# Kernel optimization log

Hardware: AMD Instinct MI355X
Metric: run time of the kernel (lower is better)

## Reference

```python
import jax, jax.numpy as jnp
import numpy as np

B, S, D_IN, D_OUT, R = 8, 2048, 4096, 4096, 16

def setup_inputs() -> dict:
    key = jax.random.key(0)
    k = jax.random.split(key, 7)
    return {
        "x": jax.random.normal(k[0], (B, S, D_IN), dtype=jnp.float32),
        "osora_U": jax.random.normal(k[1], (D_OUT, R), dtype=jnp.float32) * 0.02,
        "osora_V": jax.random.normal(k[2], (R, D_IN), dtype=jnp.float32) * 0.02,
        "osora_S": jax.random.normal(k[3], (R,), dtype=jnp.float32),
        "osora_O": jax.random.normal(k[4], (D_OUT,), dtype=jnp.float32),
        "magnitude": jax.random.uniform(k[5], (D_OUT,), dtype=jnp.float32) + 0.5,
        "base_weight": jax.random.normal(k[6], (D_OUT, D_IN), dtype=jnp.float32) * 0.02,
    }

def reference(x, osora_U, osora_V, osora_S, osora_O, magnitude, base_weight):
    # osora_weight = diag(O) @ U @ diag(S) @ V  -> [out, in]
    osora_weight = (osora_O[:, None] * (osora_U * osora_S[None, :])) @ osora_V
    # low-rank path applied to activations: x @ osora_weight.T  -> [B, S, out]
    osora_result = jnp.einsum('bsr,or->bso', jnp.einsum('bsi,ri->bsr', x, osora_V) * osora_S, osora_U) * osora_O
    # weight norm of (base + adapter) per output row; detached in the original
    weight_norm = jax.lax.stop_gradient(
        jnp.linalg.norm(base_weight + osora_weight, axis=1).astype(base_weight.dtype))
    mag_norm_scale = (magnitude / weight_norm)[None, None, :]  # broadcast over B, S
    base_out = jnp.einsum('bsi,oi->bso', x, base_weight)
    return (mag_norm_scale - 1.0) * base_out + mag_norm_scale * osora_result
```

## Files before the change

kernel.cpp:

```cpp
#include <hip/hip_runtime.h>


#define M_TOT 16384
#define N_TOT 4096
#define K_TOT 4096

typedef __attribute__((ext_vector_type(8))) short bf16x8;
typedef __attribute__((ext_vector_type(4))) float f32x4;

__device__ __forceinline__ unsigned short f2bf(float f){
  union { float f; unsigned int u; } v; v.f = f;
  unsigned int u = v.u;
  u += 0x7FFFu + ((u >> 16) & 1u);
  return (unsigned short)(u >> 16);
}

__device__ __forceinline__ void async_lds16(const void* g, void* l){
  __builtin_amdgcn_global_load_lds(
      (const __attribute__((address_space(1))) unsigned int*)g,
      (__attribute__((address_space(3))) unsigned int*)l, 16, 0, 0);
}

__global__ __launch_bounds__(256) void cast_f32_to_bf16_x4(
    const float* __restrict__ src, unsigned short* __restrict__ dst, int n4){
  int i = blockIdx.x * 256 + threadIdx.x;
  if (i >= n4) return;
  float4 v = ((const float4*)src)[i];
  ushort4 o;
  o.x = f2bf(v.x); o.y = f2bf(v.y); o.z = f2bf(v.z); o.w = f2bf(v.w);
  ((ushort4*)dst)[i] = o;
}

__global__ __launch_bounds__(256) void tgemm_kernel(
    const unsigned short* __restrict__ xb, const unsigned short* __restrict__ vb,
    unsigned short* __restrict__ tb){
  int lane = threadIdx.x & 63;
  int wave = threadIdx.x >> 6;
  int quad = lane >> 4;
  int r16  = lane & 15;
  int m0 = (blockIdx.x * 4 + wave) * 16;
  const unsigned short* xptr = xb + (m0 + r16) * K_TOT + quad * 8;
  const unsigned short* vptr = vb + r16 * K_TOT + quad * 8;
  f32x4 acc = {0.f, 0.f, 0.f, 0.f};
  for (int k = 0; k < K_TOT; k += 32){
    bf16x8 a = *(const bf16x8*)(xptr + k);
    bf16x8 b = *(const bf16x8*)(vptr + k);
    acc = __builtin_amdgcn_mfma_f32_16x16x32_bf16(a, b, acc, 0, 0, 0);
  }
  for (int reg = 0; reg < 4; reg++){
    int m = m0 + quad * 4 + reg;
    tb[m * 16 + r16] = f2bf(acc[reg]);
  }
}

__global__ __launch_bounds__(256) void norm_kernel(
    const float* __restrict__ bw, const float* __restrict__ U,
    const float* __restrict__ S, const float* __restrict__ O,
    const float* __restrict__ mag, const float* __restrict__ V,
    float* __restrict__ s_out, float* __restrict__ sm1_out,
    unsigned short* __restrict__ w2b){
  __shared__ float Vl[16 * 1024];
  __shared__ float C8[8 * 16];
  __shared__ float red[8 * 4];
  int t = threadIdx.x;
  int lane = t & 63, wave = t >> 6;
  int n0 = blockIdx.x * 8;
  if (t < 128){
    int row = t >> 4, r = t & 15;
    int n = n0 + row;
    float c = O[n] * S[r] * U[n * 16 + r];
    C8[t] = c;
    w2b[n * 16 + r] = f2bf(c);
  }
  float nsq[8];
  for (int i = 0; i < 8; i++) nsq[i] = 0.f;
  for (int ch = 0; ch < 4; ch++){
    __syncthreads();
    for (int j = 0; j < 16; j++){
      int idx4 = j * 256 + t;
      int r = idx4 >> 8, c4 = idx4 & 255;
      *(float4*)(Vl + r * 1024 + c4 * 4) =
          *(const float4*)(V + r * 4096 + ch * 1024 + c4 * 4);
    }
    __syncthreads();
    for (int row = 0; row < 8; row++){
      float4 b = *(const float4*)(bw + (n0 + row) * 4096 + ch * 1024 + t * 4);
      float a0 = 0.f, a1 = 0.f, a2 = 0.f, a3 = 0.f;
      for (int r = 0; r < 16; r++){
        float cr = C8[row * 16 + r];
        const float* vp = Vl + r * 1024 + t * 4;
        a0 += cr * vp[0]; a1 += cr * vp[1]; a2 += cr * vp[2]; a3 += cr * vp[3];
      }
      float d0 = b.x + a0, d1 = b.y + a1, d2 = b.z + a2, d3 = b.w + a3;
      nsq[row] += d0*d0 + d1*d1 + d2*d2 + d3*d3;
    }
  }
  for (int row = 0; row < 8; row++){
    float v = nsq[row];
    for (int off = 32; off > 0; off >>= 1) v += __shfl_down(v, off);
    if (lane == 0) red[row * 4 + wave] = v;
  }
  __syncthreads();
  if (t < 8){
    int n = n0 + t;
    float tot = red[t*4] + red[t*4+1] + red[t*4+2] + red[t*4+3];
    float s = mag[n] / sqrtf(tot);
    s_out[n] = s;
    sm1_out[n] = s - 1.0f;
  }
}

__global__ __launch_bounds__(256) void gemm_kernel(
    const unsigned short* __restrict__ A,
    const unsigned short* __restrict__ B,
    const unsigned short* __restrict__ Tb,
    const unsigned short* __restrict__ W2b,
    const float* __restrict__ s_arr, const float* __restrict__ sm1_arr,
    float* __restrict__ Cout){
  __shared__ unsigned short Al[128 * 64];
  __shared__ unsigned short Bl[128 * 64];
  int tid  = threadIdx.x;
  int lane = tid & 63;
  int wave = tid >> 6;
  int quad = lane >> 4;
  int r16  = lane & 15;
  int xm   = lane & 7;

  const int GM = 16, NBN = 32;
  int bidx  = blockIdx.x;
  int super = bidx / (GM * NBN);
  int rem   = bidx % (GM * NBN);
  int bm = super * GM + (rem & (GM - 1));
  int bn = rem / GM;
  int m0 = bm * 128;
  int n0 = bn * 128;

  int wm = (wave >> 1) * 64;
  int wn = (wave & 1) * 64;

  int a_goff[4], b_goff[4], l_off[4];
  for (int j = 0; j < 4; j++){
    int u = j * 256 + tid;
    int mrow = u >> 3;
    int ko = (u & 7) ^ (mrow & 7);
    a_goff[j] = (m0 + mrow) * K_TOT + ko * 8;
    b_goff[j] = (n0 + mrow) * K_TOT + ko * 8;
    l_off[j]  = u * 8;
  }
  int koff0 = (quad ^ xm) * 16;
  int koff1 = ((4 + quad) ^ xm) * 16;

  f32x4 zf = {0.f, 0.f, 0.f, 0.f};
  f32x4 acc[4][4];
  for (int i = 0; i < 4; i++)
    for (int j = 0; j < 4; j++) acc[i][j] = zf;

  for (int kk = 0; kk < K_TOT; kk += 64){
    __syncthreads();
    for (int j = 0; j < 4; j++){
      async_lds16(A + a_goff[j] + kk, Al + l_off[j]);
      async_lds16(B + b_goff[j] + kk, Bl + l_off[j]);
    }
    __syncthreads();
    for (int ks = 0; ks < 2; ks++){
      int ko = ks ? koff1 : koff0;
      bf16x8 af[4], bfr[4];
      for (int tm = 0; tm < 4; tm++)
        af[tm] = *(const bf16x8*)((const char*)Al + (wm + tm*16 + r16) * 128 + ko);
      for (int tn = 0; tn < 4; tn++)
        bfr[tn] = *(const bf16x8*)((const char*)Bl + (wn + tn*16 + r16) * 128 + ko);
      for (int tm = 0; tm < 4; tm++)
        for (int tn = 0; tn < 4; tn++)
          acc[tm][tn] = __builtin_amdgcn_mfma_f32_16x16x32_bf16(
              af[tm], bfr[tn], acc[tm][tn], 0, 0, 0);
    }
  }

  __syncthreads();
  {
    int row = tid >> 1, half = tid & 1;
    uint4 z = {0u, 0u, 0u, 0u};
    *(uint4*)(Al + row * 40 + half * 8)      = *(const uint4*)(Tb  + (m0 + row) * 16 + half * 8);
    *(uint4*)(Al + row * 40 + 16 + half * 8) = z;
    *(uint4*)(Bl + row * 40 + half * 8)      = *(const uint4*)(W2b + (n0 + row) * 16 + half * 8);
    *(uint4*)(Bl + row * 40 + 16 + half * 8) = z;
  }
  __syncthreads();
  for (int tn = 0; tn < 4; tn++){
    int nn = n0 + wn + tn * 16 + r16;
    float s   = s_arr[nn];
    float sm1 = sm1_arr[nn];
    bf16x8 b2 = *(const bf16x8*)(Bl + (wn + tn*16 + r16) * 40 + quad * 8);
    for (int tm = 0; tm < 4; tm++){
      bf16x8 a2 = *(const bf16x8*)(Al + (wm + tm*16 + r16) * 40 + quad * 8);
      f32x4 o2 = __builtin_amdgcn_mfma_f32_16x16x32_bf16(a2, b2, zf, 0, 0, 0);
      int mbase = m0 + wm + tm * 16 + quad * 4;
      float* cp = Cout + (long)mbase * N_TOT + nn;
      cp[0]         = sm1 * acc[tm][tn][0] + s * o2[0];
      cp[N_TOT]     = sm1 * acc[tm][tn][1] + s * o2[1];
      cp[2 * N_TOT] = sm1 * acc[tm][tn][2] + s * o2[2];
      cp[3 * N_TOT] = sm1 * acc[tm][tn][3] + s * o2[3];
    }
  }
}

extern "C" void kernel_launch(void* const* d_in, const int* in_sizes, int n_in,
                              void* d_out, int out_size, void* d_ws, size_t ws_size,
                              hipStream_t stream){
  const float* x   = (const float*)d_in[0];
  const float* U   = (const float*)d_in[1];
  const float* V   = (const float*)d_in[2];
  const float* S   = (const float*)d_in[3];
  const float* O   = (const float*)d_in[4];
  const float* mag = (const float*)d_in[5];
  const float* bw  = (const float*)d_in[6];
  float* out = (float*)d_out;

  char* ws = (char*)d_ws;
  unsigned short* xb  = (unsigned short*)(ws);
  unsigned short* wb  = (unsigned short*)(ws + 134217728);
  unsigned short* vb  = (unsigned short*)(ws + 167772160);
  unsigned short* tb  = (unsigned short*)(ws + 167903232);
  unsigned short* w2b = (unsigned short*)(ws + 168427520);
  float* s_arr   = (float*)(ws + 168558592);
  float* sm1_arr = (float*)(ws + 168574976);
  (void)in_sizes; (void)n_in; (void)out_size; (void)ws_size;

  cast_f32_to_bf16_x4<<<16384, 256, 0, stream>>>(bw, wb, 4194304);
  cast_f32_to_bf16_x4<<<64,    256, 0, stream>>>(V,  vb, 16384);
  cast_f32_to_bf16_x4<<<65536, 256, 0, stream>>>(x,  xb, 16777216);
  tgemm_kernel<<<256, 256, 0, stream>>>(xb, vb, tb);
  norm_kernel<<<512, 256, 0, stream>>>(bw, U, S, O, mag, V, s_arr, sm1_arr, w2b);
  gemm_kernel<<<4096, 256, 0, stream>>>(xb, wb, tb, w2b, s_arr, sm1_arr, out);
}
```

Before: 1.271 ms.

## Rewrite main GEMM as 256x256 tile with double-buffered ping-pong LDS pipeline

The fused GEMM moves from 128x128 tiles with 4 waves to 256x256 tiles with 8 waves. LDS is double-buffered, and async global-to-LDS loads for the next K-step are issued between MFMA clusters. Explicit vmcnt/lgkmcnt waits, barriers and s_setprio interleave memory traffic with MFMA work, and the block order is remapped for L2 reuse. The aim is to hide global-load latency and raise arithmetic intensity. The cost is 128KB of LDS per block, many barriers, and high register pressure from the 8x4 accumulator array.

After: 1.081 ms. 15.0% less time.

```diff
diff --git a/kernel.cpp b/kernel.cpp
--- a/kernel.cpp
+++ b/kernel.cpp
@@ -110,98 +110,169 @@
   }
 }
 
-__global__ __launch_bounds__(256) void gemm_kernel(
+__global__ __launch_bounds__(512, 2) void gemm_kernel(
     const unsigned short* __restrict__ A,
     const unsigned short* __restrict__ B,
     const unsigned short* __restrict__ Tb,
     const unsigned short* __restrict__ W2b,
     const float* __restrict__ s_arr, const float* __restrict__ sm1_arr,
     float* __restrict__ Cout){
-  __shared__ unsigned short Al[128 * 64];
-  __shared__ unsigned short Bl[128 * 64];
+  __shared__ unsigned short AL[2][16384];
+  __shared__ unsigned short BL[2][16384];
   int tid  = threadIdx.x;
   int lane = tid & 63;
   int wave = tid >> 6;
+  int wm   = wave >> 2;
+  int wn   = wave & 3;
   int quad = lane >> 4;
   int r16  = lane & 15;
-  int xm   = lane & 7;
-
-  const int GM = 16, NBN = 32;
-  int bidx  = blockIdx.x;
-  int super = bidx / (GM * NBN);
-  int rem   = bidx % (GM * NBN);
-  int bm = super * GM + (rem & (GM - 1));
-  int bn = rem / GM;
-  int m0 = bm * 128;
-  int n0 = bn * 128;
-
-  int wm = (wave >> 1) * 64;
-  int wn = (wave & 1) * 64;
-
-  int a_goff[4], b_goff[4], l_off[4];
-  for (int j = 0; j < 4; j++){
-    int u = j * 256 + tid;
-    int mrow = u >> 3;
-    int ko = (u & 7) ^ (mrow & 7);
-    a_goff[j] = (m0 + mrow) * K_TOT + ko * 8;
-    b_goff[j] = (n0 + mrow) * K_TOT + ko * 8;
-    l_off[j]  = u * 8;
-  }
-  int koff0 = (quad ^ xm) * 16;
-  int koff1 = ((4 + quad) ^ xm) * 16;
+  int xm   = r16 & 7;
+
+  int bid = blockIdx.x;
+  int id  = (bid & 7) * 128 + (bid >> 3);
+  int bm = id >> 4, bn = id & 15;
+  int m0 = bm * 256, n0 = bn * 256;
+
+  int urow0 = tid >> 3,         uslot0 = tid & 7;
+  int urow1 = (512+tid) >> 3,   uslot1 = (512+tid) & 7;
+  int ko0 = uslot0 ^ (urow0 & 7);
+  int ko1 = uslot1 ^ (urow1 & 7);
+  int a_src0 = (m0 + urow0) * K_TOT + ko0 * 8;
+  int a_src1 = (m0 + urow1) * K_TOT + ko1 * 8;
+  int b_src0 = (n0 + urow0) * K_TOT + ko0 * 8;
+  int b_src1 = (n0 + urow1) * K_TOT + ko1 * 8;
+  int l_u0 = tid * 8;
+  int l_u1 = (512 + tid) * 8;
+  const int HSTEP = 128 * K_TOT;
+
+#define STG_A(bf_, h_, kt_) do{ \
+    async_lds16(A + a_src0 + (h_)*HSTEP + (kt_)*64, &AL[bf_][(h_)*8192 + l_u0]); \
+    async_lds16(A + a_src1 + (h_)*HSTEP + (kt_)*64, &AL[bf_][(h_)*8192 + l_u1]); }while(0)
+#define STG_B(bf_, h_, kt_) do{ \
+    async_lds16(B + b_src0 + (h_)*HSTEP + (kt_)*64, &BL[bf_][(h_)*8192 + l_u0]); \
+    async_lds16(B + b_src1 + (h_)*HSTEP + (kt_)*64, &BL[bf_][(h_)*8192 + l_u1]); }while(0)
+
+#define BAR()   __builtin_amdgcn_s_barrier()
+#define LGKM0() asm volatile("s_waitcnt lgkmcnt(0)" ::: "memory")
+#define VMW(n_) asm volatile("s_waitcnt vmcnt(" #n_ ")" ::: "memory")
+
+  int a_row = (wm * 128 + r16) * 64;
+  int b_row = (wn * 64  + r16) * 64;
+  int koA[2] = { (quad ^ xm) * 8, ((4 + quad) ^ xm) * 8 };
 
   f32x4 zf = {0.f, 0.f, 0.f, 0.f};
-  f32x4 acc[4][4];
-  for (int i = 0; i < 4; i++)
+  f32x4 acc[8][4];
+#pragma unroll
+  for (int i = 0; i < 8; i++)
+#pragma unroll
     for (int j = 0; j < 4; j++) acc[i][j] = zf;
-
-  for (int kk = 0; kk < K_TOT; kk += 64){
-    __syncthreads();
-    for (int j = 0; j < 4; j++){
-      async_lds16(A + a_goff[j] + kk, Al + l_off[j]);
-      async_lds16(B + b_goff[j] + kk, Bl + l_off[j]);
-    }
-    __syncthreads();
-    for (int ks = 0; ks < 2; ks++){
-      int ko = ks ? koff1 : koff0;
-      bf16x8 af[4], bfr[4];
-      for (int tm = 0; tm < 4; tm++)
-        af[tm] = *(const bf16x8*)((const char*)Al + (wm + tm*16 + r16) * 128 + ko);
-      for (int tn = 0; tn < 4; tn++)
-        bfr[tn] = *(const bf16x8*)((const char*)Bl + (wn + tn*16 + r16) * 128 + ko);
-      for (int tm = 0; tm < 4; tm++)
-        for (int tn = 0; tn < 4; tn++)
-          acc[tm][tn] = __builtin_amdgcn_mfma_f32_16x16x32_bf16(
-              af[tm], bfr[tn], acc[tm][tn], 0, 0, 0);
-    }
-  }
-
+  bf16x8 af[4][2], bA[2][2], bB[2][2];
+
+#define RD_A(bf_, mb_) do{ _Pragma("unroll") \
+    for (int mf = 0; mf < 4; ++mf){ _Pragma("unroll") \
+      for (int ks = 0; ks < 2; ++ks) \
+        af[mf][ks] = *(const bf16x8*)(&AL[bf_][a_row + ((mb_)+mf)*1024 + koA[ks]]); } }while(0)
+#define RD_B(bf_, dst_, nb_) do{ _Pragma("unroll") \
+    for (int nf = 0; nf < 2; ++nf){ _Pragma("unroll") \
+      for (int ks = 0; ks < 2; ++ks) \
+        dst_[nf][ks] = *(const bf16x8*)(&BL[bf_][b_row + ((nb_)+nf)*1024 + koA[ks]]); } }while(0)
+#define MMQ(mb_, bset_, nb_) do{ _Pragma("unroll") \
+    for (int ks = 0; ks < 2; ++ks){ _Pragma("unroll") \
+      for (int mf = 0; mf < 4; ++mf){ _Pragma("unroll") \
+        for (int nf = 0; nf < 2; ++nf) \
+          acc[(mb_)+mf][(nb_)+nf] = __builtin_amdgcn_mfma_f32_16x16x32_bf16( \
+              af[mf][ks], bset_[nf][ks], acc[(mb_)+mf][(nb_)+nf], 0, 0, 0); } } }while(0)
+
+  STG_A(0, 0, 0); STG_A(0, 1, 0); STG_B(0, 0, 0); STG_B(0, 1, 0);
+  STG_B(1, 0, 1); STG_B(1, 1, 1); STG_A(1, 0, 1);
+  VMW(6);
+  BAR();
+
+#pragma unroll 1
+  for (int i = 0; i < 32; ++i){
+    int kt = 2 * i;
+    int pf = (i < 31);
+
+    RD_A(0, 0); RD_B(0, bA, 0);
+    STG_A(1, 1, kt + 1);
+    BAR(); LGKM0();
+    __builtin_amdgcn_s_setprio(1); MMQ(0, bA, 0); __builtin_amdgcn_s_setprio(0);
+    BAR();
+    RD_B(0, bB, 2);
+    BAR(); LGKM0();
+    __builtin_amdgcn_s_setprio(1); MMQ(0, bB, 2); __builtin_amdgcn_s_setprio(0);
+    BAR();
+    RD_A(0, 4);
+    if (pf) STG_B(0, 0, kt + 2);
+    BAR(); LGKM0();
+    __builtin_amdgcn_s_setprio(1); MMQ(4, bA, 0); __builtin_amdgcn_s_setprio(0);
+    BAR();
+    if (pf) STG_B(0, 1, kt + 2);
+    BAR(); LGKM0();
+    __builtin_amdgcn_s_setprio(1); MMQ(4, bB, 2); __builtin_amdgcn_s_setprio(0);
+    if (pf) { VMW(4); } else { VMW(0); }
+    BAR();
+    RD_A(1, 0); RD_B(1, bA, 0);
+    if (pf) STG_A(0, 0, kt + 2);
+    BAR(); LGKM0();
+    __builtin_amdgcn_s_setprio(1); MMQ(0, bA, 0); __builtin_amdgcn_s_setprio(0);
+    BAR();
+    RD_B(1, bB, 2);
+    if (pf) STG_A(0, 1, kt + 2);
+    BAR(); LGKM0();
+    __builtin_amdgcn_s_setprio(1); MMQ(0, bB, 2); __builtin_amdgcn_s_setprio(0);
+    BAR();
+    RD_A(1, 4);
+    if (pf) STG_B(1, 0, kt + 3);
+    BAR(); LGKM0();
+    __builtin_amdgcn_s_setprio(1); MMQ(4, bA, 0); __builtin_amdgcn_s_setprio(0);
+    BAR();
+    if (pf) { STG_B(1, 1, kt + 3); STG_A(1, 0, kt + 3); }
+    BAR(); LGKM0();
+    __builtin_amdgcn_s_setprio(1); MMQ(4, bB, 2); __builtin_amdgcn_s_setprio(0);
+    VMW(6);
+    BAR();
+  }
+
+  VMW(0);
   __syncthreads();
   {
     int row = tid >> 1, half = tid & 1;
     uint4 z = {0u, 0u, 0u, 0u};
-    *(uint4*)(Al + row * 40 + half * 8)      = *(const uint4*)(Tb  + (m0 + row) * 16 + half * 8);
-    *(uint4*)(Al + row * 40 + 16 + half * 8) = z;
-    *(uint4*)(Bl + row * 40 + half * 8)      = *(const uint4*)(W2b + (n0 + row) * 16 + half * 8);
-    *(uint4*)(Bl + row * 40 + 16 + half * 8) = z;
+    unsigned short* Tp = &AL[0][0];
+    unsigned short* Wp = &BL[0][0];
+    *(uint4*)(Tp + row * 40 + half * 8)      = *(const uint4*)(Tb  + (m0 + row) * 16 + half * 8);
+    *(uint4*)(Tp + row * 40 + 16 + half * 8) = z;
+    *(uint4*)(Wp + row * 40 + half * 8)      = *(const uint4*)(W2b + (n0 + row) * 16 + half * 8);
+    *(uint4*)(Wp + row * 40 + 16 + half * 8) = z;
   }
   __syncthreads();
-  for (int tn = 0; tn < 4; tn++){
-    int nn = n0 + wn + tn * 16 + r16;
+#pragma unroll
+  for (int nf = 0; nf < 4; ++nf){
+    int nn = n0 + wn * 64 + nf * 16 + r16;
     float s   = s_arr[nn];
     float sm1 = sm1_arr[nn];
-    bf16x8 b2 = *(const bf16x8*)(Bl + (wn + tn*16 + r16) * 40 + quad * 8);
-    for (int tm = 0; tm < 4; tm++){
-      bf16x8 a2 = *(const bf16x8*)(Al + (wm + tm*16 + r16) * 40 + quad * 8);
+    bf16x8 b2 = *(const bf16x8*)(&BL[0][(wn * 64 + nf * 16 + r16) * 40 + quad * 8]);
+#pragma unroll
+    for (int mf = 0; mf < 8; ++mf){
+      bf16x8 a2 = *(const bf16x8*)(&AL[0][(wm * 128 + mf * 16 + r16) * 40 + quad * 8]);
       f32x4 o2 = __builtin_amdgcn_mfma_f32_16x16x32_bf16(a2, b2, zf, 0, 0, 0);
-      int mbase = m0 + wm + tm * 16 + quad * 4;
+      int mbase = m0 + wm * 128 + mf * 16 + quad * 4;
       float* cp = Cout + (long)mbase * N_TOT + nn;
-      cp[0]         = sm1 * acc[tm][tn][0] + s * o2[0];
-      cp[N_TOT]     = sm1 * acc[tm][tn][1] + s * o2[1];
-      cp[2 * N_TOT] = sm1 * acc[tm][tn][2] + s * o2[2];
-      cp[3 * N_TOT] = sm1 * acc[tm][tn][3] + s * o2[3];
+      cp[0]         = sm1 * acc[mf][nf][0] + s * o2[0];
+      cp[N_TOT]     = sm1 * acc[mf][nf][1] + s * o2[1];
+      cp[2 * N_TOT] = sm1 * acc[mf][nf][2] + s * o2[2];
+      cp[3 * N_TOT] = sm1 * acc[mf][nf][3] + s * o2[3];
     }
   }
+#undef STG_A
+#undef STG_B
+#undef RD_A
+#undef RD_B
+#undef MMQ
+#undef BAR
+#undef LGKM0
+#undef VMW
 }
 
 extern "C" void kernel_launch(void* const* d_in, const int* in_sizes, int n_in,
@@ -231,5 +302,5 @@
   cast_f32_to_bf16_x4<<<65536, 256, 0, stream>>>(x,  xb, 16777216);
   tgemm_kernel<<<256, 256, 0, stream>>>(xb, vb, tb);
   norm_kernel<<<512, 256, 0, stream>>>(bw, U, S, O, mag, V, s_arr, sm1_arr, w2b);
-  gemm_kernel<<<4096, 256, 0, stream>>>(xb, wb, tb, w2b, s_arr, sm1_arr, out);
-}
+  gemm_kernel<<<1024, 512, 0, stream>>>(xb, wb, tb, w2b, s_arr, sm1_arr, out);
+}
```
